# Optimization experiments

Hardware: AMD Instinct MI355X
Metric: run time of the kernel (lower is better)

Reference implementation:

```python
import jax, jax.numpy as jnp
from jax import lax
import numpy as np

B, N, T = 16, 1024, 12
H_DIM, D_FF, NHEADS = 64, 256, 4
SDIM, DDIM, WDIM = 32, 16, 15
D_IN = 1 + SDIM + DDIM + WDIM  # 64


def setup_inputs() -> dict:
    key = jax.random.key(0)
    ks = jax.random.split(key, 32)
    def p(k, shape, s=0.05):
        return jax.random.normal(k, shape, dtype=jnp.float32) * s
    h = H_DIM
    inp = {
        'flow': jax.random.normal(ks[0], (B, N, T), dtype=jnp.float32),
        'day_idx': jax.random.randint(ks[1], (B, N, T), 0, 288),
        'week_idx': jax.random.randint(ks[2], (B, N, T), 0, 7),
        'spatial_emb': p(ks[3], (N, SDIM)),
        'daily_emb': p(ks[4], (288, DDIM)),
        'weekly_emb': p(ks[5], (7, WDIM)),
        'gfs_fc_w': p(ks[6], (h, D_IN)), 'gfs_fc_b': jnp.zeros(h),
        'glu_w': p(ks[7], (2 * h, h)), 'glu_b': jnp.zeros(2 * h),
        'gc_weight': p(ks[8], (h, h)),
        'gc_A': p(ks[9], (N, N), 0.02), 'gc_A2': p(ks[10], (N, N), 0.02),
        'ds_init_w': p(ks[11], (2 * h, h, 1, 3)), 'ds_init_b': jnp.zeros(2 * h),
        'ds_p1m_w': p(ks[12], (h, h, 1, 3)), 'ds_p1m_b': jnp.zeros(h),
        'ds_p1g_w': p(ks[13], (h, h, 1, 3)), 'ds_p1g_b': jnp.zeros(h),
        'ds_p2m_w': p(ks[14], (h, h, 1, 3)), 'ds_p2m_b': jnp.zeros(h),
        'ds_p2g_w': p(ks[15], (h, h, 1, 3)), 'ds_p2g_b': jnp.zeros(h),
        'ds_fc_w': p(ks[16], (h, 2 * h)), 'ds_fc_b': jnp.zeros(h),
        'wq': p(ks[17], (h, h)), 'bq': jnp.zeros(h),
        'wk': p(ks[18], (h, h)), 'bk': jnp.zeros(h),
        'wv': p(ks[19], (h, h)), 'bv': jnp.zeros(h),
        'wo': p(ks[20], (h, h)), 'bo': jnp.zeros(h),
        'ff1_w': p(ks[21], (D_FF, h)), 'ff1_b': jnp.zeros(D_FF),
        'ff2_w': p(ks[22], (h, D_FF)), 'ff2_b': jnp.zeros(h),
        'ln1_g': jnp.ones(h), 'ln1_b': jnp.zeros(h),
        'ln2_g': jnp.ones(h), 'ln2_b': jnp.zeros(h),
        'cl_w': p(ks[23], (T,)), 'cl_b': jnp.zeros(()),
    }
    return inp


def _ln(x, g, b):
    m = jnp.mean(x, -1, keepdims=True)
    v = jnp.mean(jnp.square(x - m), -1, keepdims=True)
    return (x - m) * lax.rsqrt(v + 1e-5) * g + b


def _conv1xk(x, w, b):
    # x: [B, C, N, T], w: [O, I, 1, 3], padding (0,1) along time
    y = lax.conv_general_dilated(x, w, (1, 1), ((0, 0), (1, 1)),
                                 dimension_numbers=('NCHW', 'OIHW', 'NCHW'))
    return y + b[None, :, None, None]


def reference(flow, day_idx, week_idx, spatial_emb, daily_emb, weekly_emb,
              gfs_fc_w, gfs_fc_b, glu_w, glu_b, gc_weight, gc_A, gc_A2,
              ds_init_w, ds_init_b, ds_p1m_w, ds_p1m_b, ds_p1g_w, ds_p1g_b,
              ds_p2m_w, ds_p2m_b, ds_p2g_w, ds_p2g_b, ds_fc_w, ds_fc_b,
              wq, bq, wk, bk, wv, bv, wo, bo, ff1_w, ff1_b, ff2_w, ff2_b,
              ln1_g, ln1_b, ln2_g, ln2_b, cl_w, cl_b):
    h = H_DIM
    # --- InfoEmb: concat flow + spatial + daily + weekly embeddings ---
    sp = jnp.broadcast_to(spatial_emb[None, :, None, :], (B, N, T, SDIM))
    x = jnp.concatenate([flow[..., None], sp, daily_emb[day_idx], weekly_emb[week_idx]], -1)  # [B,N,T,64]
    # --- GFS: 1x1 conv + GLU (channels == last dim) ---
    x = x @ gfs_fc_w.T + gfs_fc_b
    g = x @ glu_w.T + glu_b
    lhs, rhs = g[..., :h], g[..., h:]
    x = lhs * jax.nn.sigmoid(rhs)  # [B,N,T,h]
    # --- TASTGC: adaptive spatial graph conv with two learned adjacencies ---
    A1 = jax.nn.softmax(jax.nn.relu(gc_A), axis=1)
    A2 = jax.nn.softmax(jax.nn.relu(gc_A2), axis=1)
    hs = jnp.einsum('mn,bntd->bmtd', A1, x) + jnp.einsum('mn,bntd->bmtd', A2, x)
    x = jax.nn.relu(jnp.einsum('bntd,de->bnte', hs, gc_weight))  # [B,N,T,h]
    # --- DSFIN: dual-path gated temporal conv ---
    xd = jnp.transpose(x, (0, 3, 1, 2))  # [B,h,N,T]
    x_init = _conv1xk(xd, ds_init_w, ds_init_b)  # [B,2h,N,T]
    p1, p2 = x_init[:, :h], x_init[:, h:]
    p1o = _conv1xk(p1, ds_p1m_w, ds_p1m_b) * jax.nn.sigmoid(_conv1xk(p1, ds_p1g_w, ds_p1g_b))
    p2o = _conv1xk(p2, ds_p2m_w, ds_p2m_b) * jax.nn.sigmoid(_conv1xk(p2, ds_p2g_w, ds_p2g_b))
    fused = jax.nn.relu(jnp.concatenate([p1o, p2o], 1) + x_init)  # [B,2h,N,T]
    fused = jnp.transpose(fused, (0, 2, 3, 1))  # [B,N,T,2h]
    x = fused @ ds_fc_w.T + ds_fc_b  # [B,N,T,h]
    # --- EncoderLayer: multi-head attention along time per node ---
    dk = h // NHEADS
    y = x.reshape(B * N, T, h)
    q = (y @ wq.T + bq).reshape(B * N, T, NHEADS, dk)
    k = (y @ wk.T + bk).reshape(B * N, T, NHEADS, dk)
    v = (y @ wv.T + bv).reshape(B * N, T, NHEADS, dk)
    scores = jnp.einsum('blhd,bshd->bhls', q, k) / jnp.sqrt(jnp.float32(dk))
    attn = jax.nn.softmax(scores, -1)
    o = jnp.einsum('bhls,bshd->blhd', attn, v).reshape(B * N, T, h)
    y1 = _ln(y + (o @ wo.T + bo), ln1_g, ln1_b)
    ff = jax.nn.relu(y1 @ ff1_w.T + ff1_b) @ ff2_w.T + ff2_b
    y2 = _ln(y1 + ff, ln2_g, ln2_b).reshape(B, N, T, h)
    # --- CongestionLearn: symmetric sigmoid node-node gate from flow ---
    f = jax.nn.relu(flow @ cl_w + cl_b)  # [B,N]
    m = jnp.mean(f, 0)  # [N]
    fuse = jax.nn.sigmoid((m[:, None] + m[None, :]) * 0.5)  # [N,N]
    out = jnp.einsum('mn,bntd->bmtd', fuse, y2)  # [B,N,T,h]
    return out
```

## Files before the change

### kernel.cpp

```cpp
#include <hip/hip_runtime.h>
#include <hip/hip_bf16.h>
#include <cstdint>

#define B_ 16
#define N_ 1024
#define T_ 12
#define HD 64
#define BN_ (B_*N_)
#define BNT (B_*N_*T_)
#define TD (T_*HD)

typedef __attribute__((ext_vector_type(8))) short short8;
typedef __attribute__((ext_vector_type(4))) float f32x4;

#define MFMA16(a,b,c) __builtin_amdgcn_mfma_f32_16x16x32_bf16(a,b,c,0,0,0)

__device__ __forceinline__ float sigmoidf_(float x) { return 1.f / (1.f + __expf(-x)); }

__device__ __forceinline__ unsigned short f2bf(float f) {
  __hip_bfloat16 h = __float2bfloat16(f);
  return __builtin_bit_cast(unsigned short, h);
}
__device__ __forceinline__ unsigned int f2bf2(float lo, float hi) {
  return (unsigned int)f2bf(lo) | ((unsigned int)f2bf(hi) << 16);
}
__device__ __forceinline__ float bf2f(unsigned short h) {
  unsigned int u = ((unsigned int)h) << 16;
  return __uint_as_float(u);
}

__device__ __forceinline__ float blkRedMax(float v, float* red) {
  #pragma unroll
  for (int off = 32; off >= 1; off >>= 1) v = fmaxf(v, __shfl_xor(v, off));
  int w = threadIdx.x >> 6;
  if ((threadIdx.x & 63) == 0) red[w] = v;
  __syncthreads();
  v = fmaxf(fmaxf(red[0], red[1]), fmaxf(red[2], red[3]));
  __syncthreads();
  return v;
}
__device__ __forceinline__ float blkRedSum(float v, float* red) {
  #pragma unroll
  for (int off = 32; off >= 1; off >>= 1) v += __shfl_xor(v, off);
  int w = threadIdx.x >> 6;
  if ((threadIdx.x & 63) == 0) red[w] = v;
  __syncthreads();
  v = red[0] + red[1] + red[2] + red[3];
  __syncthreads();
  return v;
}

__global__ void k_wprep_all(
    const float* __restrict__ w1, const float* __restrict__ w2, const float* __restrict__ gcw,
    const float* __restrict__ wi,
    const float* __restrict__ w1m, const float* __restrict__ w1g,
    const float* __restrict__ w2m, const float* __restrict__ w2g,
    const float* __restrict__ wfc,
    const float* __restrict__ wq, const float* __restrict__ wk,
    const float* __restrict__ wv, const float* __restrict__ wo,
    const float* __restrict__ f1w, const float* __restrict__ f2w,
    unsigned short* __restrict__ wTe, unsigned short* __restrict__ wds,
    unsigned short* __restrict__ wat)
{
  int t = blockIdx.x*256 + threadIdx.x;
  if (t < 4096)        wat[t] = f2bf(wq[t]);
  else if (t < 8192)   wat[t] = f2bf(wk[t-4096]);
  else if (t < 12288)  wat[t] = f2bf(wv[t-8192]);
  else if (t < 16384)  wat[t] = f2bf(wo[t-12288]);
  else if (t < 32768)  wat[t] = f2bf(f1w[t-16384]);
  else                 wat[t] = f2bf(f2w[t-32768]);
  if (t < 4096)       wTe[t] = f2bf(w1[t]);
  else if (t < 12288) wTe[t] = f2bf(w2[t-4096]);
  else if (t < 16384) {
    int r = t - 12288, e = r >> 6, d = r & 63;
    wTe[12288 + e*64 + d] = f2bf(gcw[d*64 + e]);
  }
  if (t < 24576) {
    int o = t / 192, k = t - o*192, tap = k >> 6, i = k & 63;
    wds[o*192 + k] = f2bf(wi[(o*64 + i)*3 + tap]);
  }
  if (t < 12288) {
    int o = t / 192, k = t - o*192, tap = k >> 6, i = k & 63;
    int src = (o*64 + i)*3 + tap;
    wds[24576 + o*192 + k]      = f2bf(w1m[src]);
    wds[24576 + (64+o)*192 + k] = f2bf(w1g[src]);
    wds[49152 + o*192 + k]      = f2bf(w2m[src]);
    wds[49152 + (64+o)*192 + k] = f2bf(w2g[src]);
  }
  if (t < 8192) wds[73728 + t] = f2bf(wfc[t]);
}

__global__ __launch_bounds__(256) void k_embed3(
    const float* __restrict__ flow, const int* __restrict__ day, const int* __restrict__ week,
    const float* __restrict__ semb, const float* __restrict__ demb, const float* __restrict__ wemb,
    const unsigned short* __restrict__ wTe, const float* __restrict__ b1,
    const float* __restrict__ b2,
    unsigned short* __restrict__ outw)
{
  __shared__ unsigned short sEa[128*72];
  __shared__ unsigned short sEb[128*72];
  const unsigned short* W1  = wTe;
  const unsigned short* W2  = wTe + 4096;
  const unsigned short* GcT = wTe + 12288;

  int tid = threadIdx.x, lane = tid & 63, w = tid >> 6;
  int l15 = lane & 15, l4 = lane >> 4;
  int row0 = blockIdx.x * 128;

  for (int i = tid; i < 8192; i += 256) {
    int r = i >> 6, c = i & 63;
    int row = row0 + r;
    int n = (row / T_) & (N_-1);
    float val;
    if (c == 0)      val = flow[row];
    else if (c < 33) val = semb[n*32 + (c-1)];
    else if (c < 49) val = demb[day[row]*16 + (c-33)];
    else             val = wemb[week[row]*15 + (c-49)];
    sEa[r*72 + c] = f2bf(val);
  }
  __syncthreads();

  {
    f32x4 acc[8] = {};
    #pragma unroll
    for (int ks = 0; ks < 2; ++ks) {
      short8 bf = *(const short8*)&W1[(w*16 + l15)*64 + ks*32 + l4*8];
      #pragma unroll
      for (int mt = 0; mt < 8; ++mt) {
        short8 af = *(const short8*)&sEa[(mt*16 + l15)*72 + ks*32 + l4*8];
        acc[mt] = MFMA16(af, bf, acc[mt]);
      }
    }
    float bias = b1[w*16 + l15];
    #pragma unroll
    for (int mt = 0; mt < 8; ++mt)
      #pragma unroll
      for (int r = 0; r < 4; ++r)
        sEb[(mt*16 + l4*4 + r)*72 + w*16 + l15] = f2bf(acc[mt][r] + bias);
  }
  __syncthreads();

  {
    f32x4 alo[8] = {}, ahi[8] = {};
    #pragma unroll
    for (int ks = 0; ks < 2; ++ks) {
      short8 blo = *(const short8*)&W2[(size_t)(w*16 + l15)*64 + ks*32 + l4*8];
      short8 bhi = *(const short8*)&W2[(size_t)(64 + w*16 + l15)*64 + ks*32 + l4*8];
      #pragma unroll
      for (int mt = 0; mt < 8; ++mt) {
        short8 af = *(const short8*)&sEb[(mt*16 + l15)*72 + ks*32 + l4*8];
        alo[mt] = MFMA16(af, blo, alo[mt]);
        ahi[mt] = MFMA16(af, bhi, ahi[mt]);
      }
    }
    float blov = b2[w*16 + l15], bhiv = b2[64 + w*16 + l15];
    #pragma unroll
    for (int mt = 0; mt < 8; ++mt)
      #pragma unroll
      for (int r = 0; r < 4; ++r) {
        float v = (alo[mt][r] + blov) * sigmoidf_(ahi[mt][r] + bhiv);
        sEa[(mt*16 + l4*4 + r)*72 + w*16 + l15] = f2bf(v);
      }
  }
  __syncthreads();

  {
    f32x4 acc[8] = {};
    #pragma unroll
    for (int ks = 0; ks < 2; ++ks) {
      short8 bf = *(const short8*)&GcT[(w*16 + l15)*64 + ks*32 + l4*8];
      #pragma unroll
      for (int mt = 0; mt < 8; ++mt) {
        short8 af = *(const short8*)&sEa[(mt*16 + l15)*72 + ks*32 + l4*8];
        acc[mt] = MFMA16(af, bf, acc[mt]);
      }
    }
    #pragma unroll
    for (int mt = 0; mt < 8; ++mt)
      #pragma unroll
      for (int r = 0; r < 4; ++r)
        outw[(size_t)(row0 + mt*16 + l4*4 + r)*64 + w*16 + l15] = f2bf(acc[mt][r]);
  }
}

__global__ __launch_bounds__(256) void k_aprep(
    const float* __restrict__ A1, const float* __restrict__ A2, unsigned short* __restrict__ Aout)
{
  __shared__ float red[4];
  int m = blockIdx.x, tid = threadIdx.x;
  float mx0, is0, mx1, is1;
  {
    const float* src = A1 + (size_t)m*N_;
    float mx = 0.f;
    for (int i = tid; i < N_; i += 256) mx = fmaxf(mx, fmaxf(src[i], 0.f));
    mx = blkRedMax(mx, red);
    float s = 0.f;
    for (int i = tid; i < N_; i += 256) s += __expf(fmaxf(src[i], 0.f) - mx);
    s = blkRedSum(s, red);
    mx0 = mx; is0 = 1.f / s;
  }
  {
    const float* src = A2 + (size_t)m*N_;
    float mx = 0.f;
    for (int i = tid; i < N_; i += 256) mx = fmaxf(mx, fmaxf(src[i], 0.f));
    mx = blkRedMax(mx, red);
    float s = 0.f;
    for (int i = tid; i < N_; i += 256) s += __expf(fmaxf(src[i], 0.f) - mx);
    s = blkRedSum(s, red);
    mx1 = mx; is1 = 1.f / s;
  }
  const float* s1 = A1 + (size_t)m*N_;
  const float* s2 = A2 + (size_t)m*N_;
  for (int i = tid; i < N_; i += 256) {
    float v1 = __expf(fmaxf(s1[i], 0.f) - mx0) * is0;
    float v2 = __expf(fmaxf(s2[i], 0.f) - mx1) * is1;
    Aout[(size_t)m*N_ + i] = f2bf(v1 + v2);
  }
}

template<int RELU, int OB16>
__global__ __launch_bounds__(256) void k_gemm_mfma(
    const unsigned short* __restrict__ A, const unsigned short* __restrict__ X,
    void* __restrict__ C, int K, int P)
{
  __shared__ unsigned short sA[128*40];
  __shared__ unsigned short sB[128*40];
  int tid = threadIdx.x, lane = tid & 63, wid = tid >> 6;
  int M = gridDim.y * 128;
  int b = blockIdx.z;
  const unsigned short* Xb = X + (size_t)b*K*P;
  int m0 = blockIdx.y*128, p0 = blockIdx.x*128;
  int wr = wid >> 1, wc = wid & 1;

  f32x4 acc[4][4] = {};

  for (int k0 = 0; k0 < K; k0 += 32) {
    #pragma unroll
    for (int pass = 0; pass < 2; ++pass) {
      int r = (tid >> 2) + 64*pass, kk = (tid & 3)*8;
      short8 v = *(const short8*)&A[(size_t)(m0+r)*K + k0 + kk];
      *(short8*)&sA[r*40 + kk] = v;
    }
    #pragma unroll
    for (int pass = 0; pass < 4; ++pass) {
      int p  = (tid & 63) + 64*(pass & 1);
      int k4 = (tid >> 6)*4 + 16*(pass >> 1);
      ushort4 h;
      h.x = Xb[(size_t)(k0+k4+0)*P + p0 + p];
      h.y = Xb[(size_t)(k0+k4+1)*P + p0 + p];
      h.z = Xb[(size_t)(k0+k4+2)*P + p0 + p];
      h.w = Xb[(size_t)(k0+k4+3)*P + p0 + p];
      *(ushort4*)&sB[p*40 + k4] = h;
    }
    __syncthreads();
    short8 af[4], bf[4];
    #pragma unroll
    for (int f = 0; f < 4; ++f) {
      af[f] = *(const short8*)&sA[(wr*64 + f*16 + (lane & 15))*40 + (lane >> 4)*8];
      bf[f] = *(const short8*)&sB[(wc*64 + f*16 + (lane & 15))*40 + (lane >> 4)*8];
    }
    #pragma unroll
    for (int fm = 0; fm < 4; ++fm)
      #pragma unroll
      for (int fn = 0; fn < 4; ++fn)
        acc[fm][fn] = MFMA16(af[fm], bf[fn], acc[fm][fn]);
    __syncthreads();
  }
  #pragma unroll
  for (int fm = 0; fm < 4; ++fm) {
    int row = m0 + wr*64 + fm*16 + (lane >> 4)*4;
    #pragma unroll
    for (int fn = 0; fn < 4; ++fn) {
      int col = p0 + wc*64 + fn*16 + (lane & 15);
      #pragma unroll
      for (int r = 0; r < 4; ++r) {
        float v = acc[fm][fn][r];
        if (RELU) v = fmaxf(v, 0.f);
        if (OB16) {
          unsigned short* Cb = (unsigned short*)C + (size_t)b*M*P;
          Cb[(size_t)(row + r)*P + col] = f2bf(v);
        } else {
          float* Cb = (float*)C + (size_t)b*M*P;
          Cb[(size_t)(row + r)*P + col] = v;
        }
      }
    }
  }
}

__global__ __launch_bounds__(256) void k_ds3(
    const unsigned short* xds,
    const unsigned short* __restrict__ Wall,
    const float* __restrict__ bi,
    const float* __restrict__ b1m, const float* __restrict__ b1g,
    const float* __restrict__ b2m, const float* __restrict__ b2g,
    const float* __restrict__ bfc,
    unsigned short* outg)
{
  __shared__ unsigned short smem[36352];
  unsigned short* X_lds  = smem;
  unsigned short* xi_lds = smem + 8064;
  unsigned short* fu_lds = smem + 23296;
  const unsigned short* WiB  = Wall;
  const unsigned short* Wg1B = Wall + 24576;
  const unsigned short* Wg2B = Wall + 49152;
  const unsigned short* WfB  = Wall + 73728;

  int tid = threadIdx.x, lane = tid & 63, wid = tid >> 6;
  int l15 = lane & 15, l4 = lane >> 4;
  int bn0 = blockIdx.x * 8;

  for (int i = tid; i < 8*2*72; i += 256) {
    int g = i / 144, r = i - g*144;
    int tp = (r < 72) ? 0 : 13, c = (r < 72) ? r : r - 72;
    X_lds[(g*14 + tp)*72 + c] = 0;
  }
  for (int i = tid; i < 8*2*136; i += 256) {
    int g = i / 272, r = i - g*272;
    int tp = (r < 136) ? 0 : 13, c = (r < 136) ? r : r - 136;
    xi_lds[(g*14 + tp)*136 + c] = 0;
  }
  for (int i = tid; i < 768; i += 256) {
    int g = i / 96, rem = i - g*96, t = rem >> 3, i8 = rem & 7;
    short8 v = *(const short8*)&xds[(size_t)(bn0+g)*768 + t*64 + i8*8];
    *(short8*)&X_lds[(g*14 + t + 1)*72 + i8*8] = v;
  }
  __syncthreads();

  int ga[6], ta[6];
  #pragma unroll
  for (int mt = 0; mt < 6; ++mt) {
    int r = mt*16 + l15;
    ga[mt] = r / 12; ta[mt] = r - ga[mt]*12;
  }

  {
    f32x4 acc1[6][2] = {};
    int nb = wid*2;
    #pragma unroll
    for (int ks = 0; ks < 6; ++ks) {
      int tap = ks >> 1, i0 = (ks & 1)*32;
      short8 af[6];
      #pragma unroll
      for (int mt = 0; mt < 6; ++mt)
        af[mt] = *(const short8*)&X_lds[(ga[mt]*14 + ta[mt] + tap)*72 + i0 + l4*8];
      short8 bf0 = *(const short8*)&WiB[(size_t)((nb  )*16 + l15)*192 + ks*32 + l4*8];
      short8 bf1 = *(const short8*)&WiB[(size_t)((nb+1)*16 + l15)*192 + ks*32 + l4*8];
      #pragma unroll
      for (int mt = 0; mt < 6; ++mt) {
        acc1[mt][0] = MFMA16(af[mt], bf0, acc1[mt][0]);
        acc1[mt][1] = MFMA16(af[mt], bf1, acc1[mt][1]);
      }
    }
    #pragma unroll
    for (int nn = 0; nn < 2; ++nn) {
      int o = (nb+nn)*16 + l15;
      float bv = bi[o];
      #pragma unroll
      for (int mt = 0; mt < 6; ++mt) {
        #pragma unroll
        for (int reg = 0; reg < 4; ++reg) {
          int r = mt*16 + l4*4 + reg;
          int g = r / 12, t = r - g*12;
          xi_lds[(g*14 + t + 1)*136 + o] = f2bf(acc1[mt][nn][reg] + bv);
        }
      }
    }
  }
  __syncthreads();

  #pragma unroll
  for (int h = 0; h < 2; ++h) {
    const unsigned short* Wg = h ? Wg2B : Wg1B;
    f32x4 am[6] = {}, ag[6] = {};
    #pragma unroll
    for (int ks = 0; ks < 6; ++ks) {
      int tap = ks >> 1, i0 = (ks & 1)*32;
      short8 af[6];
      #pragma unroll
      for (int mt = 0; mt < 6; ++mt)
        af[mt] = *(const short8*)&xi_lds[(ga[mt]*14 + ta[mt] + tap)*136 + h*64 + i0 + l4*8];
      short8 bm = *(const short8*)&Wg[(size_t)(wid*16 + l15)*192 + ks*32 + l4*8];
      short8 bg = *(const short8*)&Wg[(size_t)((wid+4)*16 + l15)*192 + ks*32 + l4*8];
      #pragma unroll
      for (int mt = 0; mt < 6; ++mt) {
        am[mt] = MFMA16(af[mt], bm, am[mt]);
        ag[mt] = MFMA16(af[mt], bg, ag[mt]);
      }
    }
    int o = wid*16 + l15;
    float bmv = (h ? b2m : b1m)[o];
    float bgv = (h ? b2g : b1g)[o];
    #pragma unroll
    for (int mt = 0; mt < 6; ++mt) {
      #pragma unroll
      for (int reg = 0; reg < 4; ++reg) {
        int r = mt*16 + l4*4 + reg;
        int g = r / 12, t = r - g*12;
        float pm = am[mt][reg] + bmv;
        float pg = ag[mt][reg] + bgv;
        float po = pm * sigmoidf_(pg);
        float xi = bf2f(xi_lds[(g*14 + t + 1)*136 + h*64 + o]);
        fu_lds[r*136 + h*64 + o] = f2bf(fmaxf(po + xi, 0.f));
      }
    }
  }
  __syncthreads();

  {
    f32x4 a3[6] = {};
    #pragma unroll
    for (int ks = 0; ks < 4; ++ks) {
      short8 af = *(const short8*)&WfB[(size_t)(wid*16 + l15)*128 + ks*32 + l4*8];
      #pragma unroll
      for (int nt = 0; nt < 6; ++nt) {
        short8 bf = *(const short8*)&fu_lds[(nt*16 + l15)*136 + ks*32 + l4*8];
        a3[nt] = MFMA16(af, bf, a3[nt]);
      }
    }
    int e0 = wid*16 + l4*4;
    float4 bb = *(const float4*)&bfc[e0];
    #pragma unroll
    for (int nt = 0; nt < 6; ++nt) {
      uint2 vv;
      vv.x = f2bf2(a3[nt][0] + bb.x, a3[nt][1] + bb.y);
      vv.y = f2bf2(a3[nt][2] + bb.z, a3[nt][3] + bb.w);
      *(uint2*)&outg[((size_t)(bn0 + ga[nt])*12 + ta[nt])*64 + e0] = vv;
    }
  }
}

__global__ __launch_bounds__(512) void k_attn4(
    const unsigned short* __restrict__ xg,
    const unsigned short* __restrict__ Wat,
    const float* __restrict__ bq, const float* __restrict__ bk, const float* __restrict__ bv,
    const float* __restrict__ bo,
    const float* __restrict__ f1b, const float* __restrict__ f2b,
    const float* __restrict__ g1, const float* __restrict__ be1,
    const float* __restrict__ g2, const float* __restrict__ be2,
    unsigned short* __restrict__ outg)
{
  __shared__ unsigned short su[36864];
  __shared__ float part[2][4][96];
  __shared__ float stats[2][96];
  unsigned short* Ybuf = su;
  unsigned short* Qkv  = su + 6912;
  unsigned short* Hb   = su + 6912;
  unsigned short* atts = su + 33792;

  const unsigned short* Wqkv = Wat;
  const unsigned short* Wo   = Wat + 12288;
  const unsigned short* F1   = Wat + 16384;
  const unsigned short* F2   = Wat + 32768;

  int tid = threadIdx.x, lane = tid & 63, w = tid >> 6;
  int l15 = lane & 15, l4 = lane >> 4;
  int wn = w & 3, wm = w >> 2;
  size_t base = (size_t)blockIdx.x * 8 * 768;

  for (int i = tid; i < 768; i += 512) {
    int r = i >> 3, c = i & 7;
    *(short8*)&Ybuf[r*72 + c*8] = *(const short8*)&xg[base + r*64 + c*8];
  }
  __syncthreads();

  {
    short8 afA[2][3], bfA[2][3];
    #pragma unroll
    for (int ks = 0; ks < 2; ++ks) {
      #pragma unroll
      for (int ni = 0; ni < 3; ++ni)
        bfA[ks][ni] = *(const short8*)&Wqkv[(size_t)((wn*3+ni)*16 + l15)*64 + ks*32 + l4*8];
      #pragma unroll
      for (int mi = 0; mi < 3; ++mi)
        afA[ks][mi] = *(const short8*)&Ybuf[((wm*3+mi)*16 + l15)*72 + ks*32 + l4*8];
    }
    f32x4 acc[3][3] = {};
    #pragma unroll
    for (int ks = 0; ks < 2; ++ks)
      #pragma unroll
      for (int ni = 0; ni < 3; ++ni)
        #pragma unroll
        for (int mi = 0; mi < 3; ++mi)
          acc[mi][ni] = MFMA16(afA[ks][mi], bfA[ks][ni], acc[mi][ni]);
    #pragma unroll
    for (int ni = 0; ni < 3; ++ni) {
      int col = (wn*3+ni)*16 + l15;
      float bias = col < 64 ? bq[col] : (col < 128 ? bk[col-64] : bv[col-128]);
      #pragma unroll
      for (int mi = 0; mi < 3; ++mi)
        #pragma unroll
        for (int r = 0; r < 4; ++r)
          Qkv[((wm*3+mi)*16 + l4*4 + r)*216 + col] = f2bf(acc[mi][ni][r] + bias);
    }
  }
  __syncthreads();

  {
    int rb = w*12;
    unsigned short* as = atts + w*384;
    #pragma unroll
    for (int h = 0; h < 4; ++h) {
      short8 kf = {}, qf = {};
      if (l4 < 2) {
        kf = *(const short8*)&Qkv[(rb + l15)*216 + 64 + h*16 + l4*8];
        qf = *(const short8*)&Qkv[(rb + l15)*216 +      h*16 + l4*8];
      }
      f32x4 sc = {};
      sc = MFMA16(kf, qf, sc);
      float e[4]; float mx = -3e38f;
      #pragma unroll
      for (int r = 0; r < 4; ++r) {
        float v = (l4 == 3) ? -3e38f : sc[r]*0.25f;
        e[r] = v; mx = fmaxf(mx, v);
      }
      mx = fmaxf(mx, __shfl_xor(mx, 16));
      mx = fmaxf(mx, __shfl_xor(mx, 32));
      float s = 0.f;
      #pragma unroll
      for (int r = 0; r < 4; ++r) { e[r] = __expf(e[r] - mx); s += e[r]; }
      s += __shfl_xor(s, 16); s += __shfl_xor(s, 32);
      float inv = 1.f/s;
      uint2 pk = make_uint2(f2bf2(e[0]*inv, e[1]*inv), f2bf2(e[2]*inv, e[3]*inv));
      *(uint2*)&as[l15*24 + l4*4] = pk;
      short8 aaf = {};
      if (l4 < 2) aaf = *(const short8*)&as[l15*24 + l4*8];
      short8 vf = {};
      if (l4 < 2) {
        #pragma unroll
        for (int j = 0; j < 8; ++j) {
          int s_ = l4*8 + j;
          vf[j] = (s_ < 12) ? (short)Qkv[(rb + s_)*216 + 128 + h*16 + l15] : (short)0;
        }
      }
      f32x4 o = {};
      o = MFMA16(aaf, vf, o);
      if (l4 < 3) {
        #pragma unroll
        for (int r = 0; r < 4; ++r)
          Qkv[(rb + l4*4 + r)*216 + h*16 + l15] = f2bf(o[r]);
      }
    }
  }
  __syncthreads();

  {
    short8 bfA[2], afA[2][3];
    #pragma unroll
    for (int ks = 0; ks < 2; ++ks) {
      bfA[ks] = *(const short8*)&Wo[(size_t)(wn*16 + l15)*64 + ks*32 + l4*8];
      #pragma unroll
      for (int mi = 0; mi < 3; ++mi)
        afA[ks][mi] = *(const short8*)&Qkv[((wm*3+mi)*16 + l15)*216 + ks*32 + l4*8];
    }
    f32x4 zacc[3] = {};
    #pragma unroll
    for (int ks = 0; ks < 2; ++ks)
      #pragma unroll
      for (int mi = 0; mi < 3; ++mi)
        zacc[mi] = MFMA16(afA[ks][mi], bfA[ks], zacc[mi]);
    int col = wn*16 + l15;
    float bias = bo[col];
    #pragma unroll
    for (int mi = 0; mi < 3; ++mi)
      #pragma unroll
      for (int r = 0; r < 4; ++r) {
        int row = (wm*3+mi)*16 + l4*4 + r;
        float z = zacc[mi][r] + bias + bf2f(Ybuf[row*72 + col]);
        zacc[mi][r] = z;
        float s1 = z, s2 = z*z;
        #pragma unroll
        for (int off = 1; off <= 8; off <<= 1) { s1 += __shfl_xor(s1, off); s2 += __shfl_xor(s2, off); }
        if (l15 == 0) { part[0][wn][row] = s1; part[1][wn][row] = s2; }
      }
    __syncthreads();
    if (tid < 96) {
      float s = part[0][0][tid]+part[0][1][tid]+part[0][2][tid]+part[0][3][tid];
      float q = part[1][0][tid]+part[1][1][tid]+part[1][2][tid]+part[1][3][tid];
      float mu = s * (1.f/64.f);
      float var = q * (1.f/64.f) - mu*mu;
      stats[0][tid] = mu; stats[1][tid] = rsqrtf(var + 1e-5f);
    }
    __syncthreads();
    float gv = g1[col], bvv = be1[col];
    #pragma unroll
    for (int mi = 0; mi < 3; ++mi)
      #pragma unroll
      for (int r = 0; r < 4; ++r) {
        int row = (wm*3+mi)*16 + l4*4 + r;
        Ybuf[row*72 + col] = f2bf((zacc[mi][r] - stats[0][row]) * stats[1][row] * gv + bvv);
      }
  }
  __syncthreads();

  {
    short8 afA[2][3], bfA[2][4];
    #pragma unroll
    for (int ks = 0; ks < 2; ++ks) {
      #pragma unroll
      for (int i = 0; i < 4; ++i)
        bfA[ks][i] = *(const short8*)&F1[(size_t)((wn*4+i)*16 + l15)*64 + ks*32 + l4*8];
      #pragma unroll
      for (int mi = 0; mi < 3; ++mi)
        afA[ks][mi] = *(const short8*)&Ybuf[((wm*3+mi)*16 + l15)*72 + ks*32 + l4*8];
    }
    f32x4 acc[3][4] = {};
    #pragma unroll
    for (int ks = 0; ks < 2; ++ks)
      #pragma unroll
      for (int i = 0; i < 4; ++i)
        #pragma unroll
        for (int mi = 0; mi < 3; ++mi)
          acc[mi][i] = MFMA16(afA[ks][mi], bfA[ks][i], acc[mi][i]);
    #pragma unroll
    for (int i = 0; i < 4; ++i) {
      int col = (wn*4+i)*16 + l15;
      float bias = f1b[col];
      #pragma unroll
      for (int mi = 0; mi < 3; ++mi)
        #pragma unroll
        for (int r = 0; r < 4; ++r)
          Hb[((wm*3+mi)*16 + l4*4 + r)*280 + col] = f2bf(fmaxf(acc[mi][i][r] + bias, 0.f));
    }
  }
  __syncthreads();

  {
    f32x4 acc[3] = {};
    #pragma unroll
    for (int half = 0; half < 2; ++half) {
      short8 bfA[4], afA[4][3];
      #pragma unroll
      for (int k2 = 0; k2 < 4; ++k2) {
        int ks = half*4 + k2;
        bfA[k2] = *(const short8*)&F2[(size_t)(wn*16 + l15)*256 + ks*32 + l4*8];
        #pragma unroll
        for (int mi = 0; mi < 3; ++mi)
          afA[k2][mi] = *(const short8*)&Hb[((wm*3+mi)*16 + l15)*280 + ks*32 + l4*8];
      }
      #pragma unroll
      for (int k2 = 0; k2 < 4; ++k2)
        #pragma unroll
        for (int mi = 0; mi < 3; ++mi)
          acc[mi] = MFMA16(afA[k2][mi], bfA[k2], acc[mi]);
    }
    int col = wn*16 + l15;
    float bias = f2b[col];
    #pragma unroll
    for (int mi = 0; mi < 3; ++mi)
      #pragma unroll
      for (int r = 0; r < 4; ++r) {
        int row = (wm*3+mi)*16 + l4*4 + r;
        float z = acc[mi][r] + bias + bf2f(Ybuf[row*72 + col]);
        acc[mi][r] = z;
        float s1 = z, s2 = z*z;
        #pragma unroll
        for (int off = 1; off <= 8; off <<= 1) { s1 += __shfl_xor(s1, off); s2 += __shfl_xor(s2, off); }
        if (l15 == 0) { part[0][wn][row] = s1; part[1][wn][row] = s2; }
      }
    __syncthreads();
    if (tid < 96) {
      float s = part[0][0][tid]+part[0][1][tid]+part[0][2][tid]+part[0][3][tid];
      float q = part[1][0][tid]+part[1][1][tid]+part[1][2][tid]+part[1][3][tid];
      float mu = s * (1.f/64.f);
      float var = q * (1.f/64.f) - mu*mu;
      stats[0][tid] = mu; stats[1][tid] = rsqrtf(var + 1e-5f);
    }
    __syncthreads();
    float gv = g2[col], bvv = be2[col];
    #pragma unroll
    for (int mi = 0; mi < 3; ++mi)
      #pragma unroll
      for (int r = 0; r < 4; ++r) {
        int row = (wm*3+mi)*16 + l4*4 + r;
        outg[base + row*64 + col] = f2bf((acc[mi][r] - stats[0][row]) * stats[1][row] * gv + bvv);
      }
  }
}

__global__ void k_mvec(const float* __restrict__ flow, const float* __restrict__ clw,
                       const float* __restrict__ clb, float* __restrict__ mv)
{
  int n = blockIdx.x*blockDim.x + threadIdx.x;
  if (n < N_) {
    float s = 0.f;
    float bias = clb[0];
    for (int b = 0; b < B_; ++b) {
      const float* f = flow + ((size_t)b*N_ + n)*T_;
      float acc = bias;
      #pragma unroll
      for (int t = 0; t < T_; ++t) acc += f[t]*clw[t];
      s += fmaxf(acc, 0.f);
    }
    mv[n] = s * (1.f/16.f);
  }
}

__global__ void k_fusemat(const float* __restrict__ mv, unsigned short* __restrict__ F)
{
  int idx = blockIdx.x*256 + threadIdx.x;
  int m = idx >> 10, n = idx & 1023;
  float x = 0.5f*(mv[m] + mv[n]);
  F[idx] = f2bf(1.f/(1.f + __expf(-x)));
}

extern "C" void kernel_launch(void* const* d_in, const int* in_sizes, int n_in,
                              void* d_out, int out_size, void* d_ws, size_t ws_size,
                              hipStream_t stream)
{
  const float* flow = (const float*)d_in[0];
  const int*   day  = (const int*)d_in[1];
  const int*   week = (const int*)d_in[2];
  const float* semb = (const float*)d_in[3];
  const float* demb = (const float*)d_in[4];
  const float* wemb = (const float*)d_in[5];
  const float* gfsw = (const float*)d_in[6];
  const float* gfsb = (const float*)d_in[7];
  const float* gluw = (const float*)d_in[8];
  const float* glub = (const float*)d_in[9];
  const float* gcw  = (const float*)d_in[10];
  const float* gcA  = (const float*)d_in[11];
  const float* gcA2 = (const float*)d_in[12];
  const float* wi   = (const float*)d_in[13];
  const float* bi   = (const float*)d_in[14];
  const float* w1m  = (const float*)d_in[15];
  const float* b1m  = (const float*)d_in[16];
  const float* w1g  = (const float*)d_in[17];
  const float* b1g  = (const float*)d_in[18];
  const float* w2m  = (const float*)d_in[19];
  const float* b2m  = (const float*)d_in[20];
  const float* w2g  = (const float*)d_in[21];
  const float* b2g  = (const float*)d_in[22];
  const float* wfc  = (const float*)d_in[23];
  const float* bfc  = (const float*)d_in[24];
  const float* wq   = (const float*)d_in[25];
  const float* bq   = (const float*)d_in[26];
  const float* wk   = (const float*)d_in[27];
  const float* bk   = (const float*)d_in[28];
  const float* wv   = (const float*)d_in[29];
  const float* bv   = (const float*)d_in[30];
  const float* wo   = (const float*)d_in[31];
  const float* bo   = (const float*)d_in[32];
  const float* f1w  = (const float*)d_in[33];
  const float* f1b  = (const float*)d_in[34];
  const float* f2w  = (const float*)d_in[35];
  const float* f2b  = (const float*)d_in[36];
  const float* g1   = (const float*)d_in[37];
  const float* be1  = (const float*)d_in[38];
  const float* g2   = (const float*)d_in[39];
  const float* be2  = (const float*)d_in[40];
  const float* clw  = (const float*)d_in[41];
  const float* clb  = (const float*)d_in[42];

  float* out = (float*)d_out;
  char* ws = (char*)d_ws;
  unsigned short* Amat = (unsigned short*)ws;
  float* mv  = (float*)(ws + (size_t)2*1024*1024);
  unsigned short* wTe = (unsigned short*)(ws + (size_t)2*1024*1024 + 64*1024);
  unsigned short* wds = (unsigned short*)(ws + (size_t)2*1024*1024 + 128*1024);
  unsigned short* wat = (unsigned short*)(ws + (size_t)2*1024*1024 + 320*1024);
  unsigned short* xw  = (unsigned short*)(ws + (size_t)3*1024*1024);
  unsigned short* xds = (unsigned short*)(ws + (size_t)28*1024*1024);

  k_wprep_all<<<192, 256, 0, stream>>>(gfsw, gluw, gcw,
                                       wi, w1m, w1g, w2m, w2g, wfc,
                                       wq, wk, wv, wo, f1w, f2w,
                                       wTe, wds, wat);
  k_embed3<<<BNT/128, 256, 0, stream>>>(flow, day, week, semb, demb, wemb,
                                        wTe, gfsb, glub, xw);
  k_aprep<<<N_, 256, 0, stream>>>(gcA, gcA2, Amat);
  dim3 gg(TD/128, N_/128, B_);
  k_gemm_mfma<1,1><<<gg, 256, 0, stream>>>(Amat, xw, xds, N_, TD);
  k_ds3<<<BN_/8, 256, 0, stream>>>(xds, wds, bi, b1m, b1g, b2m, b2g, bfc, xds);
  k_attn4<<<BN_/8, 512, 0, stream>>>(xds, wat, bq, bk, bv, bo, f1b, f2b,
                                     g1, be1, g2, be2, xw);
  k_mvec<<<N_/256, 256, 0, stream>>>(flow, clw, clb, mv);
  k_fusemat<<<(N_*N_)/256, 256, 0, stream>>>(mv, Amat);
  k_gemm_mfma<0,0><<<gg, 256, 0, stream>>>(Amat, xw, out, N_, TD);
}
```

Measured before the change: 330.4 us.

## Shrink attention kernel LDS footprint to raise occupancy

The fused attention/FFN kernel now uses much less shared memory. The FFN hidden buffer is split into two 128-wide halves with an extra barrier, the Qkv row stride is narrowed, and the softmax probability staging buffer is replaced by cross-lane shuffles. LayerNorm partial sums and stats are stored as bf16 instead of fp32, and operand fragment loads are interleaved with the MFMAs to cut register pressure. The goal is more resident blocks per CU, at the cost of extra synchronisation and reduced LayerNorm statistic precision, since sum-of-squares in bf16 risks accuracy loss.

```diff
diff --git a/kernel.cpp b/kernel.cpp
--- a/kernel.cpp
+++ b/kernel.cpp
@@ -430,7 +430,7 @@
   }
 }
 
-__global__ __launch_bounds__(512) void k_attn4(
+__global__ __launch_bounds__(512) void k_attn5(
     const unsigned short* __restrict__ xg,
     const unsigned short* __restrict__ Wat,
     const float* __restrict__ bq, const float* __restrict__ bk, const float* __restrict__ bv,
@@ -440,13 +440,11 @@
     const float* __restrict__ g2, const float* __restrict__ be2,
     unsigned short* __restrict__ outg)
 {
-  __shared__ unsigned short su[36864];
-  __shared__ float part[2][4][96];
-  __shared__ float stats[2][96];
+  __shared__ unsigned short su[26112];
+  __shared__ unsigned short partb[2][4][96];
   unsigned short* Ybuf = su;
   unsigned short* Qkv  = su + 6912;
   unsigned short* Hb   = su + 6912;
-  unsigned short* atts = su + 33792;
 
   const unsigned short* Wqkv = Wat;
   const unsigned short* Wo   = Wat + 12288;
@@ -465,24 +463,21 @@
   __syncthreads();
 
   {
-    short8 afA[2][3], bfA[2][3];
+    f32x4 acc[3][3] = {};
     #pragma unroll
     for (int ks = 0; ks < 2; ++ks) {
-      #pragma unroll
-      for (int ni = 0; ni < 3; ++ni)
-        bfA[ks][ni] = *(const short8*)&Wqkv[(size_t)((wn*3+ni)*16 + l15)*64 + ks*32 + l4*8];
+      short8 af[3];
       #pragma unroll
       for (int mi = 0; mi < 3; ++mi)
-        afA[ks][mi] = *(const short8*)&Ybuf[((wm*3+mi)*16 + l15)*72 + ks*32 + l4*8];
-    }
-    f32x4 acc[3][3] = {};
-    #pragma unroll
-    for (int ks = 0; ks < 2; ++ks)
-      #pragma unroll
-      for (int ni = 0; ni < 3; ++ni)
+        af[mi] = *(const short8*)&Ybuf[((wm*3+mi)*16 + l15)*72 + ks*32 + l4*8];
+      #pragma unroll
+      for (int ni = 0; ni < 3; ++ni) {
+        short8 bf = *(const short8*)&Wqkv[(size_t)((wn*3+ni)*16 + l15)*64 + ks*32 + l4*8];
         #pragma unroll
         for (int mi = 0; mi < 3; ++mi)
-          acc[mi][ni] = MFMA16(afA[ks][mi], bfA[ks][ni], acc[mi][ni]);
+          acc[mi][ni] = MFMA16(af[mi], bf, acc[mi][ni]);
+      }
+    }
     #pragma unroll
     for (int ni = 0; ni < 3; ++ni) {
       int col = (wn*3+ni)*16 + l15;
@@ -491,20 +486,21 @@
       for (int mi = 0; mi < 3; ++mi)
         #pragma unroll
         for (int r = 0; r < 4; ++r)
-          Qkv[((wm*3+mi)*16 + l4*4 + r)*216 + col] = f2bf(acc[mi][ni][r] + bias);
+          Qkv[((wm*3+mi)*16 + l4*4 + r)*200 + col] = f2bf(acc[mi][ni][r] + bias);
     }
   }
   __syncthreads();
 
   {
     int rb = w*12;
-    unsigned short* as = atts + w*384;
+    int src0 = (l15 + 32*l4) & 63;
+    int src1 = (src0 + 16) & 63;
     #pragma unroll
     for (int h = 0; h < 4; ++h) {
       short8 kf = {}, qf = {};
       if (l4 < 2) {
-        kf = *(const short8*)&Qkv[(rb + l15)*216 + 64 + h*16 + l4*8];
-        qf = *(const short8*)&Qkv[(rb + l15)*216 +      h*16 + l4*8];
+        kf = *(const short8*)&Qkv[(rb + l15)*200 + 64 + h*16 + l4*8];
+        qf = *(const short8*)&Qkv[(rb + l15)*200 +      h*16 + l4*8];
       }
       f32x4 sc = {};
       sc = MFMA16(kf, qf, sc);
@@ -521,16 +517,21 @@
       for (int r = 0; r < 4; ++r) { e[r] = __expf(e[r] - mx); s += e[r]; }
       s += __shfl_xor(s, 16); s += __shfl_xor(s, 32);
       float inv = 1.f/s;
-      uint2 pk = make_uint2(f2bf2(e[0]*inv, e[1]*inv), f2bf2(e[2]*inv, e[3]*inv));
-      *(uint2*)&as[l15*24 + l4*4] = pk;
+      int pk0 = (int)f2bf2(e[0]*inv, e[1]*inv);
+      int pk1 = (int)f2bf2(e[2]*inv, e[3]*inv);
+      int a0 = __shfl(pk0, src0), b0 = __shfl(pk1, src0);
+      int c0 = __shfl(pk0, src1), d0 = __shfl(pk1, src1);
       short8 aaf = {};
-      if (l4 < 2) aaf = *(const short8*)&as[l15*24 + l4*8];
+      if (l4 < 2) {
+        uint4 u = make_uint4((unsigned)a0, (unsigned)b0, (unsigned)c0, (unsigned)d0);
+        aaf = __builtin_bit_cast(short8, u);
+      }
       short8 vf = {};
       if (l4 < 2) {
         #pragma unroll
         for (int j = 0; j < 8; ++j) {
           int s_ = l4*8 + j;
-          vf[j] = (s_ < 12) ? (short)Qkv[(rb + s_)*216 + 128 + h*16 + l15] : (short)0;
+          vf[j] = (s_ < 12) ? (short)Qkv[(rb + s_)*200 + 128 + h*16 + l15] : (short)0;
         }
       }
       f32x4 o = {};
@@ -538,27 +539,23 @@
       if (l4 < 3) {
         #pragma unroll
         for (int r = 0; r < 4; ++r)
-          Qkv[(rb + l4*4 + r)*216 + h*16 + l15] = f2bf(o[r]);
-      }
-    }
-  }
-  __syncthreads();
-
-  {
-    short8 bfA[2], afA[2][3];
+          Qkv[(rb + l4*4 + r)*200 + h*16 + l15] = f2bf(o[r]);
+      }
+    }
+  }
+  __syncthreads();
+
+  {
+    f32x4 zacc[3] = {};
     #pragma unroll
     for (int ks = 0; ks < 2; ++ks) {
-      bfA[ks] = *(const short8*)&Wo[(size_t)(wn*16 + l15)*64 + ks*32 + l4*8];
-      #pragma unroll
-      for (int mi = 0; mi < 3; ++mi)
-        afA[ks][mi] = *(const short8*)&Qkv[((wm*3+mi)*16 + l15)*216 + ks*32 + l4*8];
-    }
-    f32x4 zacc[3] = {};
-    #pragma unroll
-    for (int ks = 0; ks < 2; ++ks)
-      #pragma unroll
-      for (int mi = 0; mi < 3; ++mi)
-        zacc[mi] = MFMA16(afA[ks][mi], bfA[ks], zacc[mi]);
+      short8 bf = *(const short8*)&Wo[(size_t)(wn*16 + l15)*64 + ks*32 + l4*8];
+      #pragma unroll
+      for (int mi = 0; mi < 3; ++mi) {
+        short8 af = *(const short8*)&Qkv[((wm*3+mi)*16 + l15)*200 + ks*32 + l4*8];
+        zacc[mi] = MFMA16(af, bf, zacc[mi]);
+      }
+    }
     int col = wn*16 + l15;
     float bias = bo[col];
     #pragma unroll
@@ -571,15 +568,15 @@
         float s1 = z, s2 = z*z;
         #pragma unroll
         for (int off = 1; off <= 8; off <<= 1) { s1 += __shfl_xor(s1, off); s2 += __shfl_xor(s2, off); }
-        if (l15 == 0) { part[0][wn][row] = s1; part[1][wn][row] = s2; }
+        if (l15 == 0) { partb[0][wn][row] = f2bf(s1); partb[1][wn][row] = f2bf(s2); }
       }
     __syncthreads();
     if (tid < 96) {
-      float s = part[0][0][tid]+part[0][1][tid]+part[0][2][tid]+part[0][3][tid];
-      float q = part[1][0][tid]+part[1][1][tid]+part[1][2][tid]+part[1][3][tid];
+      float s = bf2f(partb[0][0][tid])+bf2f(partb[0][1][tid])+bf2f(partb[0][2][tid])+bf2f(partb[0][3][tid]);
+      float q = bf2f(partb[1][0][tid])+bf2f(partb[1][1][tid])+bf2f(partb[1][2][tid])+bf2f(partb[1][3][tid]);
       float mu = s * (1.f/64.f);
       float var = q * (1.f/64.f) - mu*mu;
-      stats[0][tid] = mu; stats[1][tid] = rsqrtf(var + 1e-5f);
+      partb[0][0][tid] = f2bf(mu); partb[1][0][tid] = f2bf(rsqrtf(var + 1e-5f));
     }
     __syncthreads();
     float gv = g1[col], bvv = be1[col];
@@ -588,61 +585,55 @@
       #pragma unroll
       for (int r = 0; r < 4; ++r) {
         int row = (wm*3+mi)*16 + l4*4 + r;
-        Ybuf[row*72 + col] = f2bf((zacc[mi][r] - stats[0][row]) * stats[1][row] * gv + bvv);
-      }
-  }
-  __syncthreads();
-
-  {
-    short8 afA[2][3], bfA[2][4];
-    #pragma unroll
-    for (int ks = 0; ks < 2; ++ks) {
-      #pragma unroll
-      for (int i = 0; i < 4; ++i)
-        bfA[ks][i] = *(const short8*)&F1[(size_t)((wn*4+i)*16 + l15)*64 + ks*32 + l4*8];
-      #pragma unroll
-      for (int mi = 0; mi < 3; ++mi)
-        afA[ks][mi] = *(const short8*)&Ybuf[((wm*3+mi)*16 + l15)*72 + ks*32 + l4*8];
-    }
-    f32x4 acc[3][4] = {};
-    #pragma unroll
-    for (int ks = 0; ks < 2; ++ks)
-      #pragma unroll
-      for (int i = 0; i < 4; ++i)
-        #pragma unroll
-        for (int mi = 0; mi < 3; ++mi)
-          acc[mi][i] = MFMA16(afA[ks][mi], bfA[ks][i], acc[mi][i]);
-    #pragma unroll
-    for (int i = 0; i < 4; ++i) {
-      int col = (wn*4+i)*16 + l15;
-      float bias = f1b[col];
-      #pragma unroll
-      for (int mi = 0; mi < 3; ++mi)
-        #pragma unroll
-        for (int r = 0; r < 4; ++r)
-          Hb[((wm*3+mi)*16 + l4*4 + r)*280 + col] = f2bf(fmaxf(acc[mi][i][r] + bias, 0.f));
-    }
-  }
-  __syncthreads();
-
-  {
-    f32x4 acc[3] = {};
-    #pragma unroll
-    for (int half = 0; half < 2; ++half) {
-      short8 bfA[4], afA[4][3];
+        float mu = bf2f(partb[0][0][row]), rs = bf2f(partb[1][0][row]);
+        Ybuf[row*72 + col] = f2bf((zacc[mi][r] - mu) * rs * gv + bvv);
+      }
+  }
+  __syncthreads();
+
+  {
+    f32x4 acc2[3] = {};
+    #pragma unroll
+    for (int fh = 0; fh < 2; ++fh) {
+      {
+        f32x4 acc[3][2] = {};
+        #pragma unroll
+        for (int ks = 0; ks < 2; ++ks) {
+          short8 af[3];
+          #pragma unroll
+          for (int mi = 0; mi < 3; ++mi)
+            af[mi] = *(const short8*)&Ybuf[((wm*3+mi)*16 + l15)*72 + ks*32 + l4*8];
+          #pragma unroll
+          for (int i = 0; i < 2; ++i) {
+            int frow = fh*128 + (wn*2+i)*16 + l15;
+            short8 bf = *(const short8*)&F1[(size_t)frow*64 + ks*32 + l4*8];
+            #pragma unroll
+            for (int mi = 0; mi < 3; ++mi)
+              acc[mi][i] = MFMA16(af[mi], bf, acc[mi][i]);
+          }
+        }
+        #pragma unroll
+        for (int i = 0; i < 2; ++i) {
+          int cl = (wn*2+i)*16 + l15;
+          float bias = f1b[fh*128 + cl];
+          #pragma unroll
+          for (int mi = 0; mi < 3; ++mi)
+            #pragma unroll
+            for (int r = 0; r < 4; ++r)
+              Hb[((wm*3+mi)*16 + l4*4 + r)*136 + cl] = f2bf(fmaxf(acc[mi][i][r] + bias, 0.f));
+        }
+      }
+      __syncthreads();
       #pragma unroll
       for (int k2 = 0; k2 < 4; ++k2) {
-        int ks = half*4 + k2;
-        bfA[k2] = *(const short8*)&F2[(size_t)(wn*16 + l15)*256 + ks*32 + l4*8];
-        #pragma unroll
-        for (int mi = 0; mi < 3; ++mi)
-          afA[k2][mi] = *(const short8*)&Hb[((wm*3+mi)*16 + l15)*280 + ks*32 + l4*8];
-      }
-      #pragma unroll
-      for (int k2 = 0; k2 < 4; ++k2)
-        #pragma unroll
-        for (int mi = 0; mi < 3; ++mi)
-          acc[mi] = MFMA16(afA[k2][mi], bfA[k2], acc[mi]);
+        short8 bf = *(const short8*)&F2[(size_t)(wn*16 + l15)*256 + fh*128 + k2*32 + l4*8];
+        #pragma unroll
+        for (int mi = 0; mi < 3; ++mi) {
+          short8 af = *(const short8*)&Hb[((wm*3+mi)*16 + l15)*136 + k2*32 + l4*8];
+          acc2[mi] = MFMA16(af, bf, acc2[mi]);
+        }
+      }
+      if (fh == 0) __syncthreads();
     }
     int col = wn*16 + l15;
     float bias = f2b[col];
@@ -651,20 +642,20 @@
       #pragma unroll
       for (int r = 0; r < 4; ++r) {
         int row = (wm*3+mi)*16 + l4*4 + r;
-        float z = acc[mi][r] + bias + bf2f(Ybuf[row*72 + col]);
-        acc[mi][r] = z;
+        float z = acc2[mi][r] + bias + bf2f(Ybuf[row*72 + col]);
+        acc2[mi][r] = z;
         float s1 = z, s2 = z*z;
         #pragma unroll
         for (int off = 1; off <= 8; off <<= 1) { s1 += __shfl_xor(s1, off); s2 += __shfl_xor(s2, off); }
-        if (l15 == 0) { part[0][wn][row] = s1; part[1][wn][row] = s2; }
+        if (l15 == 0) { partb[0][wn][row] = f2bf(s1); partb[1][wn][row] = f2bf(s2); }
       }
     __syncthreads();
     if (tid < 96) {
-      float s = part[0][0][tid]+part[0][1][tid]+part[0][2][tid]+part[0][3][tid];
-      float q = part[1][0][tid]+part[1][1][tid]+part[1][2][tid]+part[1][3][tid];
+      float s = bf2f(partb[0][0][tid])+bf2f(partb[0][1][tid])+bf2f(partb[0][2][tid])+bf2f(partb[0][3][tid]);
+      float q = bf2f(partb[1][0][tid])+bf2f(partb[1][1][tid])+bf2f(partb[1][2][tid])+bf2f(partb[1][3][tid]);
       float mu = s * (1.f/64.f);
       float var = q * (1.f/64.f) - mu*mu;
-      stats[0][tid] = mu; stats[1][tid] = rsqrtf(var + 1e-5f);
+      partb[0][0][tid] = f2bf(mu); partb[1][0][tid] = f2bf(rsqrtf(var + 1e-5f));
     }
     __syncthreads();
     float gv = g2[col], bvv = be2[col];
@@ -673,7 +664,8 @@
       #pragma unroll
       for (int r = 0; r < 4; ++r) {
         int row = (wm*3+mi)*16 + l4*4 + r;
-        outg[base + row*64 + col] = f2bf((acc[mi][r] - stats[0][row]) * stats[1][row] * gv + bvv);
+        float mu = bf2f(partb[0][0][row]), rs = bf2f(partb[1][0][row]);
+        outg[base + row*64 + col] = f2bf((acc2[mi][r] - mu) * rs * gv + bvv);
       }
   }
 }
@@ -772,7 +764,7 @@
   dim3 gg(TD/128, N_/128, B_);
   k_gemm_mfma<1,1><<<gg, 256, 0, stream>>>(Amat, xw, xds, N_, TD);
   k_ds3<<<BN_/8, 256, 0, stream>>>(xds, wds, bi, b1m, b1g, b2m, b2g, bfc, xds);
-  k_attn4<<<BN_/8, 512, 0, stream>>>(xds, wat, bq, bk, bv, bo, f1b, f2b,
+  k_attn5<<<BN_/8, 512, 0, stream>>>(xds, wat, bq, bk, bv, bo, f1b, f2b,
                                      g1, be1, g2, be2, xw);
   k_mvec<<<N_/256, 256, 0, stream>>>(flow, clw, clb, mv);
   k_fusemat<<<(N_*N_)/256, 256, 0, stream>>>(mv, Amat);
```

Result: no change. 329.6 us (-0.2%).
